# Performance work log

Hardware: AMD Instinct MI355X
Metric: run time of the kernel (lower is better)

Reference implementation:

```python
import jax, jax.numpy as jnp
import numpy as np

CONF_THRES = 0.4
IOU_THRES = 0.45
MAX_WH = 4096.0   # class offset for non-agnostic NMS (torch code: max_wh)
K_PRE = 1024      # candidates kept for the O(K^2) NMS stage (<= max_nms=30000)
MAX_DET = 300     # max detections per image (torch default)
B, N, NC = 16, 25200, 80


def xywh2xyxy(x):
    xy, wh = x[..., :2], x[..., 2:4]
    return jnp.concatenate([xy - wh * 0.5, xy + wh * 0.5], axis=-1)


def box_iou(a, b):
    # a: [K,4], b: [K,4] in xyxy
    area_a = (a[:, 2] - a[:, 0]) * (a[:, 3] - a[:, 1])
    area_b = (b[:, 2] - b[:, 0]) * (b[:, 3] - b[:, 1])
    lt = jnp.maximum(a[:, None, :2], b[None, :, :2])
    rb = jnp.minimum(a[:, None, 2:], b[None, :, 2:])
    inter = jnp.clip(rb - lt, 0.0, None).prod(-1)
    return inter / (area_a[:, None] + area_b[None, :] - inter + 1e-7)


def _nms_single(pred, conf_logit, logit, head):
    # pred [N,85] (decoded, sigmoided), conf_logit [N,5] raw, logit [N,80] raw, head [N]
    xc = pred[:, 4] > CONF_THRES                      # objectness gate
    obj_sig = jax.nn.sigmoid(conf_logit[:, 4:5])      # [N,1]
    log_sig = jax.nn.sigmoid(logit) * obj_sig         # sel_prob == 'objclass'
    cls_scores = pred[:, 5:] * pred[:, 4:5]           # x[:,5:] *= x[:,4:5]
    box = xywh2xyxy(pred[:, :4])                      # [N,4]
    conf = cls_scores.max(axis=1)                     # best class conf
    j = cls_scores.argmax(axis=1).astype(pred.dtype)  # best class id
    valid = xc & (conf > CONF_THRES)
    score = jnp.where(valid, conf, 0.0)
    # top-K candidates (sorted descending) -> fixed-shape NMS
    top_s, top_i = jax.lax.top_k(score, K_PRE)
    valid_k = top_s > 0.0
    boxes_k = box[top_i] + j[top_i, None] * MAX_WH    # per-class box offset (agnostic=False)
    iou = box_iou(boxes_k, boxes_k)                   # [K,K]
    idx = jnp.arange(K_PRE)

    def body(i, keep):
        sup = (iou[i] > IOU_THRES) & (idx > i) & keep[i]
        return keep & ~sup

    keep = jax.lax.fori_loop(0, K_PRE, body, valid_k)
    final_score = jnp.where(keep, top_s, 0.0)
    _, sel = jax.lax.top_k(final_score, MAX_DET)      # first MAX_DET survivors
    gi = top_i[sel]
    m = (final_score[sel] > 0.0).astype(pred.dtype)[:, None]  # validity mask
    det = jnp.concatenate([box[gi], conf[gi, None], j[gi, None]], axis=1)  # [300,6] xyxy,conf,cls
    # pack: det(6) | class logits*obj(80) | obj_conf(1) | classHead(1) | valid(1) -> [300,89]
    return jnp.concatenate(
        [det * m, log_sig[gi] * m, obj_sig[gi] * m, head[gi, None] * m, m], axis=1)


def setup_inputs() -> dict:
    key = jax.random.key(0)
    k1, k2, k3, k4, k5, k6 = jax.random.split(key, 6)
    xy = jax.random.uniform(k1, (B, N, 2), jnp.float32) * 640.0
    wh = 2.0 + jax.random.uniform(k2, (B, N, 2), jnp.float32) * 198.0
    objcls = jax.random.uniform(k3, (B, N, 1 + NC), jnp.float32)
    prediction = jnp.concatenate([xy, wh, objcls], axis=-1)       # [B,N,85]
    pred_conf_logits = jax.random.normal(k4, (B, N, 5), jnp.float32)
    logits = jax.random.normal(k5, (B, N, NC), jnp.float32)
    class_head = jax.random.randint(k6, (B, N), 0, 3).astype(jnp.float32)
    return {"prediction": prediction, "pred_conf_logits": pred_conf_logits,
            "logits": logits, "class_head": class_head}


def reference(prediction, pred_conf_logits, logits, class_head):
    return jax.vmap(_nms_single)(prediction, pred_conf_logits, logits, class_head)
```

## Files before the change

### kernel.cpp

```cpp
#include <hip/hip_runtime.h>
#include <math.h>

#define BATCH 16
#define NN 25200
#define NCLS 80
#define K_PRE 1024
#define MAX_DET 300
#define CONF_T 0.4f
#define IOU_T 0.45f
#define TBIAS 0x3E000000u
#define RROWS 128
#define KITER 25

__global__ void __launch_bounds__(512) score_kernel(
    const float* __restrict__ pred, unsigned long long* __restrict__ keys) {
    const int tid = threadIdx.x;
    const int r = tid >> 2, sub = tid & 3;
    const int n = blockIdx.x * RROWS + r;
    const int b = blockIdx.y;

    float best = 0.0f;
    int bc = sub * 20;
    float obj = 0.0f;
    if (n < NN) {
        const float* row = pred + ((size_t)b * NN + n) * 85;
        obj = row[4];
        if (obj > CONF_T) {
            const float* cp = row + 5 + sub * 20;
#pragma unroll
            for (int i = 0; i < 5; ++i) {
                float4 v4 = *reinterpret_cast<const float4*>(cp + 4 * i);
                float v;
                v = v4.x * obj;
                if (v > best) { best = v; bc = sub * 20 + 4 * i + 0; }
                v = v4.y * obj;
                if (v > best) { best = v; bc = sub * 20 + 4 * i + 1; }
                v = v4.z * obj;
                if (v > best) { best = v; bc = sub * 20 + 4 * i + 2; }
                v = v4.w * obj;
                if (v > best) { best = v; bc = sub * 20 + 4 * i + 3; }
            }
        }
    }
#pragma unroll
    for (int d = 1; d < 4; d <<= 1) {
        float ov = __shfl_xor(best, d);
        int oc = __shfl_xor(bc, d);
        if (ov > best || (ov == best && oc < bc)) { best = ov; bc = oc; }
    }
    if (n < NN && sub == 0) {
        unsigned t = (obj > CONF_T && best > CONF_T)
                         ? (__float_as_uint(best) - TBIAS) : 0u;
        keys[(size_t)b * NN + n] =
            ((unsigned long long)t << 22) |
            ((unsigned long long)(unsigned)(NN - 1 - n) << 7) | (unsigned)bc;
    }
}

__global__ void __launch_bounds__(1024) fused_kernel(
    const unsigned long long* __restrict__ keys,
    const float* __restrict__ pred,
    const float* __restrict__ conf_logits,
    const float* __restrict__ logits,
    const float* __restrict__ head,
    float* __restrict__ out) {
    __shared__ unsigned sA[1024], sB[1024];
    __shared__ unsigned sBC[1024];
    __shared__ unsigned long long sKeys[2048];
    __shared__ float bx0[K_PRE], by0[K_PRE], bx1[K_PRE], by1[K_PRE],
        bar_[K_PRE], bsc[K_PRE];
    __shared__ unsigned char bcls[K_PRE];
    __shared__ unsigned short bgi[K_PRE];
    __shared__ unsigned char bkeep[K_PRE];

    const int b = blockIdx.x, tid = threadIdx.x;
    const unsigned long long* bk = keys + (size_t)b * NN;

    unsigned long long kreg[KITER];
#pragma unroll
    for (int k = 0; k < KITER; ++k) {
        int i = (k << 10) + tid;
        kreg[k] = (i < NN) ? bk[i] : 0ull;
    }

    sA[tid] = 0u;
    sBC[tid] = 0u;
    sKeys[tid] = 0ull;
    sKeys[tid + 1024] = 0ull;
    __syncthreads();
#pragma unroll
    for (int k = 0; k < KITER; ++k) {
        unsigned t = (unsigned)(kreg[k] >> 22);
        if (t) atomicAdd(&sA[t >> 15], 1u);
    }
    __syncthreads();

    unsigned* src = sA;
    unsigned* dst = sB;
    for (int off = 1; off < 1024; off <<= 1) {
        dst[tid] = src[tid] + ((tid + off < 1024) ? src[tid + off] : 0u);
        __syncthreads();
        unsigned* t2 = src; src = dst; dst = t2;
    }
    const unsigned* S = src;

#pragma unroll
    for (int k = 0; k < KITER; ++k) {
        unsigned long long key = kreg[k];
        unsigned t = (unsigned)(key >> 22);
        if (t) {
            unsigned d = t >> 15;
            unsigned base = (d < 1023u) ? S[d + 1] : 0u;
            if (base < 1024u) {
                unsigned pos = base + atomicAdd(&sBC[d], 1u);
                if (pos < 2048u) sKeys[pos] = key;
            }
        }
    }
    bcls[tid] = 255;
    bsc[tid] = 0.0f;
    bkeep[tid] = 0;
    __syncthreads();

#pragma unroll
    for (int half = 0; half < 2; ++half) {
        int i = tid + (half << 10);
        unsigned long long key = sKeys[i];
        if (key) {
            unsigned t = (unsigned)(key >> 22);
            unsigned d = t >> 15;
            unsigned seg = (d < 1023u) ? S[d + 1] : 0u;
            unsigned end = seg + sBC[d];
            if (end > 2048u) end = 2048u;
            unsigned r = seg;
            for (unsigned j = seg; j < end; ++j)
                if (sKeys[j] > key) ++r;
            if (r < 1024u) {
                int n = NN - 1 - (int)((key >> 7) & 32767u);
                const float* row = pred + ((size_t)b * NN + n) * 85;
                float x = row[0], y = row[1], w = row[2], h = row[3];
                float vx0 = x - w * 0.5f, vy0 = y - h * 0.5f;
                float vx1 = x + w * 0.5f, vy1 = y + h * 0.5f;
                bx0[r] = vx0; by0[r] = vy0; bx1[r] = vx1; by1[r] = vy1;
                bar_[r] = (vx1 - vx0) * (vy1 - vy0);
                bsc[r] = __uint_as_float(t + TBIAS);
                bcls[r] = (unsigned char)(key & 127u);
                bgi[r] = (unsigned short)n;
            }
        }
    }
    __syncthreads();

    {
        const int lane = tid & 63;
        const int wv = tid >> 6;
        unsigned char myc[16];
#pragma unroll
        for (int k = 0; k < 16; ++k) myc[k] = bcls[(k << 6) | lane];

        for (int ci = 0; ci < 5; ++ci) {
            const int c = wv + (ci << 4);
            unsigned alive = 0u;
#pragma unroll
            for (int k = 0; k < 16; ++k)
                if (myc[k] == (unsigned char)c) alive |= (1u << k);
            unsigned keptm = 0u;
            for (;;) {
                int s = alive ? ((__builtin_ctz(alive) << 6) | lane)
                              : (1 << 30);
#pragma unroll
                for (int d = 32; d; d >>= 1) {
                    int o = __shfl_xor(s, d);
                    s = o < s ? o : s;
                }
                if (s >= (1 << 30)) break;
                if ((s & 63) == lane) {
                    alive &= ~(1u << (s >> 6));
                    keptm |= (1u << (s >> 6));
                }
                float ax0 = bx0[s], ay0 = by0[s], ax1 = bx1[s], ay1 = by1[s];
                float aa = bar_[s];
                unsigned rem = alive;
                while (rem) {
                    int k = __builtin_ctz(rem);
                    rem &= rem - 1;
                    int j = (k << 6) | lane;
                    float lx = fmaxf(ax0, bx0[j]);
                    float ly = fmaxf(ay0, by0[j]);
                    float rx = fminf(ax1, bx1[j]);
                    float ry = fminf(ay1, by1[j]);
                    float iw = fmaxf(rx - lx, 0.0f);
                    float ih = fmaxf(ry - ly, 0.0f);
                    float inter = iw * ih;
                    float iou = inter / (aa + bar_[j] - inter + 1e-7f);
                    if (iou > IOU_T) alive &= ~(1u << k);
                }
            }
            while (keptm) {
                int k = __builtin_ctz(keptm);
                keptm &= keptm - 1;
                bkeep[(k << 6) | lane] = 1;
            }
        }
    }
    __syncthreads();

    int kp = (int)bkeep[tid];
    src = sA; dst = sB;
    src[tid] = (unsigned)kp;
    __syncthreads();
    for (int off = 1; off < 1024; off <<= 1) {
        dst[tid] = src[tid] + ((tid >= off) ? src[tid - off] : 0u);
        __syncthreads();
        unsigned* t2 = src; src = dst; dst = t2;
    }
    int rank = (int)src[tid] - kp;
    int kcnt = (int)src[1023];

    if (kp && rank < MAX_DET) {
        int gi = (int)bgi[tid];
        float* orow = out + ((size_t)b * MAX_DET + rank) * 89;
        orow[0] = bx0[tid]; orow[1] = by0[tid];
        orow[2] = bx1[tid]; orow[3] = by1[tid];
        orow[4] = bsc[tid];
        orow[5] = (float)bcls[tid];
        float cl = conf_logits[((size_t)b * NN + gi) * 5 + 4];
        float obj_sig = 1.0f / (1.0f + expf(-cl));
        const float4* lrow4 =
            (const float4*)(logits + ((size_t)b * NN + gi) * NCLS);
#pragma unroll 4
        for (int q = 0; q < 20; ++q) {
            float4 l4 = lrow4[q];
            orow[6 + 4 * q + 0] = obj_sig / (1.0f + expf(-l4.x));
            orow[6 + 4 * q + 1] = obj_sig / (1.0f + expf(-l4.y));
            orow[6 + 4 * q + 2] = obj_sig / (1.0f + expf(-l4.z));
            orow[6 + 4 * q + 3] = obj_sig / (1.0f + expf(-l4.w));
        }
        orow[86] = obj_sig;
        orow[87] = head[(size_t)b * NN + gi];
        orow[88] = 1.0f;
    }
    if (tid < MAX_DET && tid >= kcnt) {
        float* orow = out + ((size_t)b * MAX_DET + tid) * 89;
#pragma unroll
        for (int q = 0; q < 89; ++q) orow[q] = 0.0f;
    }
}

extern "C" void kernel_launch(void* const* d_in, const int* in_sizes, int n_in,
                              void* d_out, int out_size, void* d_ws,
                              size_t ws_size, hipStream_t stream) {
    const float* pred        = (const float*)d_in[0];
    const float* conf_logits = (const float*)d_in[1];
    const float* logits      = (const float*)d_in[2];
    const float* head        = (const float*)d_in[3];
    float* out = (float*)d_out;

    unsigned long long* keys = (unsigned long long*)d_ws;

    dim3 sgrid((NN + RROWS - 1) / RROWS, BATCH);
    score_kernel<<<sgrid, 512, 0, stream>>>(pred, keys);
    fused_kernel<<<BATCH, 1024, 0, stream>>>(keys, pred, conf_logits, logits,
                                             head, out);
}
```

Measured before the change: 337.3 us.

## Split candidate selection across many blocks with global histogram and scratch in output

```diff
diff --git a/kernel.cpp b/kernel.cpp
--- a/kernel.cpp
+++ b/kernel.cpp
@@ -10,17 +10,28 @@
 #define IOU_T 0.45f
 #define TBIAS 0x3E000000u
 #define RROWS 128
-#define KITER 25
+#define OUT_STRIDE 26700
+#define SCR_KEYS_OFF 0
+#define SCR_S_OFF    16384
+#define SCR_BC_OFF   20480
 
 __global__ void __launch_bounds__(512) score_kernel(
-    const float* __restrict__ pred, unsigned long long* __restrict__ keys) {
+    const float* __restrict__ pred, unsigned long long* __restrict__ keys,
+    unsigned* __restrict__ ghist, float* __restrict__ out) {
     const int tid = threadIdx.x;
     const int r = tid >> 2, sub = tid & 3;
     const int n = blockIdx.x * RROWS + r;
     const int b = blockIdx.y;
 
+    if (blockIdx.x == 196) {
+        unsigned* bc = (unsigned*)((char*)(out + (size_t)b * OUT_STRIDE) +
+                                   SCR_BC_OFF);
+        bc[tid] = 0u;
+        bc[tid + 512] = 0u;
+    }
+
     float best = 0.0f;
-    int bc = sub * 20;
+    int bc_i = sub * 20;
     float obj = 0.0f;
     if (n < NN) {
         const float* row = pred + ((size_t)b * NN + n) * 85;
@@ -32,69 +43,45 @@
                 float4 v4 = *reinterpret_cast<const float4*>(cp + 4 * i);
                 float v;
                 v = v4.x * obj;
-                if (v > best) { best = v; bc = sub * 20 + 4 * i + 0; }
+                if (v > best) { best = v; bc_i = sub * 20 + 4 * i + 0; }
                 v = v4.y * obj;
-                if (v > best) { best = v; bc = sub * 20 + 4 * i + 1; }
+                if (v > best) { best = v; bc_i = sub * 20 + 4 * i + 1; }
                 v = v4.z * obj;
-                if (v > best) { best = v; bc = sub * 20 + 4 * i + 2; }
+                if (v > best) { best = v; bc_i = sub * 20 + 4 * i + 2; }
                 v = v4.w * obj;
-                if (v > best) { best = v; bc = sub * 20 + 4 * i + 3; }
+                if (v > best) { best = v; bc_i = sub * 20 + 4 * i + 3; }
             }
         }
     }
 #pragma unroll
     for (int d = 1; d < 4; d <<= 1) {
         float ov = __shfl_xor(best, d);
-        int oc = __shfl_xor(bc, d);
-        if (ov > best || (ov == best && oc < bc)) { best = ov; bc = oc; }
+        int oc = __shfl_xor(bc_i, d);
+        if (ov > best || (ov == best && oc < bc_i)) { best = ov; bc_i = oc; }
     }
     if (n < NN && sub == 0) {
         unsigned t = (obj > CONF_T && best > CONF_T)
                          ? (__float_as_uint(best) - TBIAS) : 0u;
         keys[(size_t)b * NN + n] =
             ((unsigned long long)t << 22) |
-            ((unsigned long long)(unsigned)(NN - 1 - n) << 7) | (unsigned)bc;
-    }
-}
-
-__global__ void __launch_bounds__(1024) fused_kernel(
+            ((unsigned long long)(unsigned)(NN - 1 - n) << 7) |
+            (unsigned)bc_i;
+        if (t) atomicAdd(&ghist[b * 1024 + (t >> 15)], 1u);
+    }
+}
+
+__global__ void __launch_bounds__(1024) select_kernel(
     const unsigned long long* __restrict__ keys,
-    const float* __restrict__ pred,
-    const float* __restrict__ conf_logits,
-    const float* __restrict__ logits,
-    const float* __restrict__ head,
-    float* __restrict__ out) {
+    const unsigned* __restrict__ ghist, float* __restrict__ out) {
     __shared__ unsigned sA[1024], sB[1024];
-    __shared__ unsigned sBC[1024];
-    __shared__ unsigned long long sKeys[2048];
-    __shared__ float bx0[K_PRE], by0[K_PRE], bx1[K_PRE], by1[K_PRE],
-        bar_[K_PRE], bsc[K_PRE];
-    __shared__ unsigned char bcls[K_PRE];
-    __shared__ unsigned short bgi[K_PRE];
-    __shared__ unsigned char bkeep[K_PRE];
-
-    const int b = blockIdx.x, tid = threadIdx.x;
-    const unsigned long long* bk = keys + (size_t)b * NN;
-
-    unsigned long long kreg[KITER];
-#pragma unroll
-    for (int k = 0; k < KITER; ++k) {
-        int i = (k << 10) + tid;
-        kreg[k] = (i < NN) ? bk[i] : 0ull;
-    }
-
-    sA[tid] = 0u;
-    sBC[tid] = 0u;
-    sKeys[tid] = 0ull;
-    sKeys[tid + 1024] = 0ull;
-    __syncthreads();
-#pragma unroll
-    for (int k = 0; k < KITER; ++k) {
-        unsigned t = (unsigned)(kreg[k] >> 22);
-        if (t) atomicAdd(&sA[t >> 15], 1u);
-    }
-    __syncthreads();
-
+    const int c = blockIdx.x, b = blockIdx.y, tid = threadIdx.x;
+    char* scratch = (char*)(out + (size_t)b * OUT_STRIDE);
+    unsigned long long* gsk = (unsigned long long*)(scratch + SCR_KEYS_OFF);
+    unsigned* gS = (unsigned*)(scratch + SCR_S_OFF);
+    unsigned* gBC = (unsigned*)(scratch + SCR_BC_OFF);
+
+    sA[tid] = ghist[b * 1024 + tid];
+    __syncthreads();
     unsigned* src = sA;
     unsigned* dst = sB;
     for (int off = 1; off < 1024; off <<= 1) {
@@ -102,20 +89,59 @@
         __syncthreads();
         unsigned* t2 = src; src = dst; dst = t2;
     }
-    const unsigned* S = src;
-
-#pragma unroll
-    for (int k = 0; k < KITER; ++k) {
-        unsigned long long key = kreg[k];
+    if (c == 0) gS[tid] = src[tid];
+
+    int i = c * 1024 + tid;
+    if (i < NN) {
+        unsigned long long key = keys[(size_t)b * NN + i];
         unsigned t = (unsigned)(key >> 22);
         if (t) {
             unsigned d = t >> 15;
-            unsigned base = (d < 1023u) ? S[d + 1] : 0u;
+            unsigned base = (d < 1023u) ? src[d + 1] : 0u;
             if (base < 1024u) {
-                unsigned pos = base + atomicAdd(&sBC[d], 1u);
-                if (pos < 2048u) sKeys[pos] = key;
-            }
-        }
+                unsigned pos = base + atomicAdd(&gBC[d], 1u);
+                if (pos < 2048u) gsk[pos] = key;
+            }
+        }
+    }
+}
+
+__global__ void __launch_bounds__(1024) nms_out_kernel(
+    const float* __restrict__ pred, const float* __restrict__ conf_logits,
+    const float* __restrict__ logits, const float* __restrict__ head,
+    float* __restrict__ out) {
+    __shared__ unsigned sS[1024];
+    __shared__ unsigned sA[1024], sB[1024];
+    __shared__ unsigned long long skeys[2048];
+    __shared__ float bx0[K_PRE], by0[K_PRE], bx1[K_PRE], by1[K_PRE],
+        bar_[K_PRE], bsc[K_PRE];
+    __shared__ unsigned char bcls[K_PRE];
+    __shared__ unsigned short bgi[K_PRE];
+    __shared__ unsigned char bkeep[K_PRE];
+    __shared__ unsigned sel_dmin;
+
+    const int b = blockIdx.x, tid = threadIdx.x;
+    char* scratch = (char*)(out + (size_t)b * OUT_STRIDE);
+    const unsigned long long* gsk =
+        (const unsigned long long*)(scratch + SCR_KEYS_OFF);
+    const unsigned* gS = (const unsigned*)(scratch + SCR_S_OFF);
+
+    sS[tid] = gS[tid];
+    if (tid == 0) sel_dmin = 0u;
+    __syncthreads();
+    {
+        unsigned base_d = (tid < 1023) ? sS[tid + 1] : 0u;
+        if (base_d < 1024u && (tid == 0 || sS[tid] >= 1024u))
+            sel_dmin = (unsigned)tid;
+    }
+    __syncthreads();
+    const unsigned M = sS[sel_dmin];
+    const unsigned Mc = M < 2048u ? M : 2048u;
+
+#pragma unroll
+    for (int half = 0; half < 2; ++half) {
+        int i = tid + (half << 10);
+        skeys[i] = ((unsigned)i < Mc) ? gsk[i] : 0ull;
     }
     bcls[tid] = 255;
     bsc[tid] = 0.0f;
@@ -125,16 +151,16 @@
 #pragma unroll
     for (int half = 0; half < 2; ++half) {
         int i = tid + (half << 10);
-        unsigned long long key = sKeys[i];
+        unsigned long long key = skeys[i];
         if (key) {
             unsigned t = (unsigned)(key >> 22);
             unsigned d = t >> 15;
-            unsigned seg = (d < 1023u) ? S[d + 1] : 0u;
-            unsigned end = seg + sBC[d];
+            unsigned seg = (d < 1023u) ? sS[d + 1] : 0u;
+            unsigned end = sS[d];
             if (end > 2048u) end = 2048u;
             unsigned r = seg;
             for (unsigned j = seg; j < end; ++j)
-                if (sKeys[j] > key) ++r;
+                if (skeys[j] > key) ++r;
             if (r < 1024u) {
                 int n = NN - 1 - (int)((key >> 7) & 32767u);
                 const float* row = pred + ((size_t)b * NN + n) * 85;
@@ -206,7 +232,8 @@
     __syncthreads();
 
     int kp = (int)bkeep[tid];
-    src = sA; dst = sB;
+    unsigned* src = sA;
+    unsigned* dst = sB;
     src[tid] = (unsigned)kp;
     __syncthreads();
     for (int off = 1; off < 1024; off <<= 1) {
@@ -256,10 +283,16 @@
     const float* head        = (const float*)d_in[3];
     float* out = (float*)d_out;
 
-    unsigned long long* keys = (unsigned long long*)d_ws;
+    char* ws = (char*)d_ws;
+    unsigned long long* keys = (unsigned long long*)ws;
+    unsigned* ghist = (unsigned*)(ws + (size_t)BATCH * NN * 8);
+
+    hipMemsetAsync(ghist, 0, (size_t)BATCH * 1024 * sizeof(unsigned), stream);
 
     dim3 sgrid((NN + RROWS - 1) / RROWS, BATCH);
-    score_kernel<<<sgrid, 512, 0, stream>>>(pred, keys);
-    fused_kernel<<<BATCH, 1024, 0, stream>>>(keys, pred, conf_logits, logits,
-                                             head, out);
-}
+    score_kernel<<<sgrid, 512, 0, stream>>>(pred, keys, ghist, out);
+    dim3 cgrid(25, BATCH);
+    select_kernel<<<cgrid, 1024, 0, stream>>>(keys, ghist, out);
+    nms_out_kernel<<<BATCH, 1024, 0, stream>>>(pred, conf_logits, logits,
+                                               head, out);
+}
```

After: 355.3 us. +5.3%, slower.
